# Kernel optimization log

Measured on AMD Instinct MI355X. Metric: run time of the kernel, lower is better.

## Reference

```python
import jax, jax.numpy as jnp
import numpy as np

B, S, D = 16, 2048, 128

def setup_inputs() -> dict:
    key = jax.random.key(0)
    kq, kk, kv, km = jax.random.split(key, 4)
    Q = jax.random.normal(kq, (B, S, D), dtype=jnp.float32)
    K = jax.random.normal(kk, (B, S, D), dtype=jnp.float32)
    V = jax.random.normal(kv, (B, S, D), dtype=jnp.float32)
    # mask: True entries are masked out (filled with -inf), same as torch.masked_fill_
    mask = jax.random.randint(km, (B, S, S), 0, 2).astype(bool)
    return {"Q": Q, "K": K, "V": V, "mask": mask, "dk": 128}

def reference(Q, K, V, mask, dk):
    # scores: [B, S_q, S_k]
    w = jnp.einsum('bqd,bkd->bqk', Q, K)
    w = jnp.where(mask, -jnp.inf, w)
    # scale applied to masked scores (as in original: mask first, then divide);
    # -inf / scale stays -inf, so math matches exactly.
    scale = jnp.asarray(dk, w.dtype) ** 0.5
    p = jax.nn.softmax(w / scale, axis=-1)
    # context: [B, S_q, D]
    return jnp.einsum('bqk,bkd->bqd', p, V)
```

## Files before the change

### kernel.cpp

```cpp
#include <hip/hip_runtime.h>
#include <hip/hip_bf16.h>
#include <stdint.h>

typedef __attribute__((ext_vector_type(8)))  short short8;
typedef __attribute__((ext_vector_type(4)))  float floatx4;
typedef __attribute__((ext_vector_type(16))) float floatx16;

#define S_LEN 2048
#define DH    128
#define BQ    64
#define BKV   64
#define NSTEP (S_LEN / BKV)
#define SCALE 0.08838834764831845f
#define SCALE2 0.12753785429791905f
#define DTHR 11.541560327111708f

__device__ __forceinline__ float ex2(float x) { return __builtin_amdgcn_exp2f(x); }

__device__ __forceinline__ unsigned short f2b(float f) {
    union { float f; unsigned u; } v; v.f = f;
    unsigned r = v.u + 0x7fffu + ((v.u >> 16) & 1u);
    return (unsigned short)(r >> 16);
}

__device__ __forceinline__ unsigned cvt_pk(float lo, float hi) {
    unsigned r;
    asm("v_cvt_pk_bf16_f32 %0, %1, %2" : "=v"(r) : "v"(lo), "v"(hi));
    return r;
}


__global__ __launch_bounds__(256) void kfrag_make(const float* __restrict__ K,
                                                  unsigned short* __restrict__ KF)
{
    const int T = blockIdx.x, b = blockIdx.y;
    const float* Kb = K + ((size_t)b * S_LEN + T * 64) * DH;
    unsigned short* out = KF + ((size_t)(b * 32 + T)) * 1024 * 8;
    #pragma unroll
    for (int i = 0; i < 4; ++i) {
        int F = i * 256 + threadIdx.x;
        int lq = F & 31, h = (F >> 5) & 1, dsub = (F >> 6) & 7, wk = F >> 9;
        const float* src = Kb + (size_t)(wk * 32 + lq) * DH + dsub * 16 + h * 8;
        float4 a = *(const float4*)src, bb = *(const float4*)(src + 4);
        short8 f;
        f[0] = f2b(a.x);  f[1] = f2b(a.y);  f[2] = f2b(a.z);  f[3] = f2b(a.w);
        f[4] = f2b(bb.x); f[5] = f2b(bb.y); f[6] = f2b(bb.z); f[7] = f2b(bb.w);
        *(short8*)(out + (size_t)F * 8) = f;
    }
}

__global__ __launch_bounds__(256) void vfrag_make(const float* __restrict__ V,
                                                  unsigned short* __restrict__ VF)
{
    __shared__ float t[32][33];
    const int k0 = blockIdx.x * 32, d0 = blockIdx.y * 32, b = blockIdx.z;
    const int tx = threadIdx.x & 31, ty = threadIdx.x >> 5;
    const float* Vb = V + ((size_t)b * S_LEN + k0) * DH + d0;
    #pragma unroll
    for (int i = 0; i < 4; ++i)
        t[ty + 8 * i][tx] = Vb[(size_t)(ty + 8 * i) * DH + tx];
    __syncthreads();
    if (threadIdx.x < 128) {
        const int lq = threadIdx.x & 31;
        const int h  = (threadIdx.x >> 5) & 1;
        const int ks = threadIdx.x >> 6;
        const int T = k0 >> 6, wk = (k0 >> 5) & 1, ds = d0 >> 5;
        short8 f;
        #pragma unroll
        for (int e = 0; e < 8; ++e)
            f[e] = f2b(t[ks * 16 + h * 8 + e][lq]);
        unsigned short* o = VF +
            ((((((size_t)(b * 32 + T) * 4 + ds) * 2 + wk) * 2 + ks) * 2 + h) * 32 + lq) * 8;
        *(short8*)o = f;
    }
}

#define PM_OFF 34816
#define LDS_BYTES 45056

__global__ __launch_bounds__(256, 2)
void attn_fwd(const float* __restrict__ Q, const unsigned short* __restrict__ KF,
              const unsigned short* __restrict__ VF,
              const int* __restrict__ M,
              float* __restrict__ O)
{
    __shared__ __align__(128) char lds[LDS_BYTES];

    const int tid  = threadIdx.x;
    const int lane = tid & 63;
    const int w    = tid >> 6;
    const int wq   = w & 1;
    const int wk   = w >> 1;
    const int lq   = lane & 31;
    const int hi   = lane >> 5;
    const int qt   = blockIdx.x;
    const int b    = blockIdx.y;
    const int q0   = qt * BQ;

    short8 qf[8];
    {
        const float* qrow = Q + ((size_t)(b * S_LEN + q0 + wq * 32 + lq)) * DH;
        #pragma unroll
        for (int dsub = 0; dsub < 8; ++dsub) {
            const float* p = qrow + dsub * 16 + hi * 8;
            float4 a  = *(const float4*)(p);
            float4 bb = *(const float4*)(p + 4);
            short8 f;
            f[0] = f2b(a.x * SCALE2);  f[1] = f2b(a.y * SCALE2);
            f[2] = f2b(a.z * SCALE2);  f[3] = f2b(a.w * SCALE2);
            f[4] = f2b(bb.x * SCALE2); f[5] = f2b(bb.y * SCALE2);
            f[6] = f2b(bb.z * SCALE2); f[7] = f2b(bb.w * SCALE2);
            qf[dsub] = f;
        }
    }

    float m_run = -1e30f;
    float l_run = 0.f;
    floatx16 accO[4];
    #pragma unroll
    for (int i = 0; i < 4; ++i) accO[i] = (floatx16)(0.f);

    const unsigned short* KFl = KF + (((size_t)(b * 32) * 2 + wk) * 512
                                      + (size_t)hi * 32 + lq) * 8;
    const unsigned short* VFl = VF + ((((size_t)(b * 32) * 4 * 2 + wk) * 2) * 2 * 32
                                      + (size_t)hi * 32 + lq) * 8;

    const int* Mq = M + (size_t)b * S_LEN * S_LEN + (size_t)q0 * S_LEN;

    int4 mA[4], mB[4];
    short8 kfc[8], vfc[8];
    unsigned long long mgc[4];

#define LOAD_KF(T) {                                                          \
    const unsigned short* kp_ = KFl + (size_t)(T) * (2 * 512 * 8);            \
    _Pragma("unroll")                                                         \
    for (int dsub = 0; dsub < 8; ++dsub)                                      \
        kfc[dsub] = *(const short8*)(kp_ + dsub * 512);                       \
}

#define LOAD_VF(T) {                                                          \
    _Pragma("unroll")                                                         \
    for (int ds = 0; ds < 4; ++ds)                                            \
        _Pragma("unroll")                                                     \
        for (int ks = 0; ks < 2; ++ks)                                        \
            vfc[ds * 2 + ks] = *(const short8*)(VFl                           \
                + ((size_t)(T) * 16 + ds * 4 + ks) * (2 * 32 * 8));           \
}

#define LOAD_MROWS(DST, G, SB) {                                              \
    _Pragma("unroll")                                                         \
    for (int rr = 0; rr < 4; ++rr)                                            \
        DST[rr] = *(const int4*)(Mq + (size_t)(w * 16 + (SB) * 4 + rr) * S_LEN \
                                 + (G) * 256 + 4 * lane);                     \
}
#define PACK_MROWS(SRC, PBUF, SB) {                                           \
    char* pms_ = lds + PM_OFF + (PBUF) * 2560;                                \
    _Pragma("unroll")                                                         \
    for (int rr = 0; rr < 4; ++rr) {                                          \
        int4 mm = SRC[rr];                                                    \
        unsigned long long b0 = __ballot(mm.x != 0);                          \
        unsigned long long b1 = __ballot(mm.y != 0);                          \
        unsigned long long b2 = __ballot(mm.z != 0);                          \
        unsigned long long b3 = __ballot(mm.w != 0);                          \
        if (lane == 0) {                                                      \
            char* rp_ = pms_ + (w * 16 + (SB) * 4 + rr) * 40;                 \
            *(unsigned long long*)(rp_ +  0) = b0;                            \
            *(unsigned long long*)(rp_ +  8) = b1;                            \
            *(unsigned long long*)(rp_ + 16) = b2;                            \
            *(unsigned long long*)(rp_ + 24) = b3;                            \
        }                                                                     \
    }                                                                         \
}

    #pragma unroll
    for (int gg = 0; gg < 2; ++gg)
        #pragma unroll
        for (int sb = 0; sb < 4; ++sb) {
            int4 t_[4];
            LOAD_MROWS(t_, gg, sb)
            PACK_MROWS(t_, gg, sb)
        }
    __syncthreads();

#define STEP_BODY(T, TT, MNEW, MOLD) {                                        \
    LOAD_KF(T);                                                               \
    LOAD_VF(T);                                                               \
               \
    if ((T) < 24) LOAD_MROWS(MNEW, ((T) >> 2) + 2, TT)                        \
                                     \
    if ((T) >= 1 && (T) <= 24) {                                              \
        const int ps_   = ((T) - 1) & 3;                                      \
        const int pbuf_ = (((((T) - 1) >> 2) + 2) & 3);                       \
        PACK_MROWS(MOLD, pbuf_, ps_)                                          \
    }                                                                         \
                   \
    if ((TT) == 0) {                                                          \
        const char* pmb_ = lds + PM_OFF + (((T) >> 2) & 3) * 2560             \
                           + (wq * 32 + lq) * 40;                             \
        mgc[0] = *(const unsigned long long*)(pmb_ + 0);                      \
        mgc[1] = *(const unsigned long long*)(pmb_ + 8);                      \
        mgc[2] = *(const unsigned long long*)(pmb_ + 16);                     \
        mgc[3] = *(const unsigned long long*)(pmb_ + 24);                     \
    }                                                                         \
                                                                    \
    floatx16 accS = (floatx16)(0.f);                                          \
    __builtin_amdgcn_s_setprio(1);                                            \
    _Pragma("unroll")                                                         \
    for (int dsub = 0; dsub < 8; ++dsub)                                      \
        accS = __builtin_amdgcn_mfma_f32_32x32x16_bf16(                       \
                   kfc[dsub], qf[dsub], accS, 0, 0, 0);                       \
    __builtin_amdgcn_s_setprio(0);                                            \
                    \
    const int base_ = (TT) * 16 + wk * 8 + hi;                                \
    unsigned mb0 = (unsigned)(mgc[0] >> base_);                               \
    unsigned mb1 = (unsigned)(mgc[1] >> base_);                               \
    unsigned mb2 = (unsigned)(mgc[2] >> base_);                               \
    unsigned mb3 = (unsigned)(mgc[3] >> base_);                               \
    float p_[16];                                                             \
    _Pragma("unroll")                                                         \
    for (int j = 0; j < 4; ++j) {                                             \
        p_[4*j+0] = ((mb0 >> (2*j)) & 1u) ? -1e30f : accS[4*j+0];             \
        p_[4*j+1] = ((mb1 >> (2*j)) & 1u) ? -1e30f : accS[4*j+1];             \
        p_[4*j+2] = ((mb2 >> (2*j)) & 1u) ? -1e30f : accS[4*j+2];             \
        p_[4*j+3] = ((mb3 >> (2*j)) & 1u) ? -1e30f : accS[4*j+3];             \
    }                                                                         \
    float mx = p_[0];                                                         \
    _Pragma("unroll")                                                         \
    for (int r = 1; r < 16; ++r) mx = fmaxf(mx, p_[r]);                       \
    mx = fmaxf(mx, __shfl_xor(mx, 32));                                       \
    int need = __any(mx - m_run > DTHR);                                      \
    float corr = 1.0f;                                                        \
    if (need) {                                                               \
        float mn = fmaxf(m_run, mx);                                          \
        corr = ex2(m_run - mn);                                               \
        m_run = mn;                                                           \
    }                                                                         \
    float ts = 0.f;                                                           \
    _Pragma("unroll")                                                         \
    for (int r = 0; r < 16; ++r) { p_[r] = ex2(p_[r] - m_run); ts += p_[r]; } \
    ts += __shfl_xor(ts, 32);                                                 \
    if (need) {                                                               \
        l_run = l_run * corr + ts;                                            \
        _Pragma("unroll")                                                     \
        for (int ds = 0; ds < 4; ++ds) {                                      \
            floatx16 o = accO[ds];                                            \
            _Pragma("unroll")                                                 \
            for (int r = 0; r < 16; ++r) o[r] *= corr;                        \
            accO[ds] = o;                                                     \
        }                                                                     \
    } else {                                                                  \
        l_run += ts;                                                          \
    }                                                                         \
                                 \
    short8 pf[2];                                                             \
    _Pragma("unroll")                                                         \
    for (int ks = 0; ks < 2; ++ks) {                                          \
        unsigned a01 = cvt_pk(p_[8*ks+0], p_[8*ks+1]);                        \
        unsigned a23 = cvt_pk(p_[8*ks+2], p_[8*ks+3]);                        \
        unsigned b01 = cvt_pk(p_[8*ks+4], p_[8*ks+5]);                        \
        unsigned b23 = cvt_pk(p_[8*ks+6], p_[8*ks+7]);                        \
        unsigned ta01 = (unsigned)__shfl_xor((int)a01, 32);                   \
        unsigned ta23 = (unsigned)__shfl_xor((int)a23, 32);                   \
        unsigned tb01 = (unsigned)__shfl_xor((int)b01, 32);                   \
        unsigned tb23 = (unsigned)__shfl_xor((int)b23, 32);                   \
        union { unsigned u[4]; short8 v; } pu;                                \
        pu.u[0] = hi ? tb01 : a01;                                            \
        pu.u[1] = hi ? tb23 : a23;                                            \
        pu.u[2] = hi ? b01 : ta01;                                            \
        pu.u[3] = hi ? b23 : ta23;                                            \
        pf[ks] = pu.v;                                                        \
    }                                                                         \
                                                                      \
    __builtin_amdgcn_s_setprio(1);                                            \
    _Pragma("unroll")                                                         \
    for (int ds = 0; ds < 4; ++ds)                                            \
        _Pragma("unroll")                                                     \
        for (int ks = 0; ks < 2; ++ks)                                        \
            accO[ds] = __builtin_amdgcn_mfma_f32_32x32x16_bf16(               \
                           vfc[ds * 2 + ks], pf[ks], accO[ds], 0, 0, 0);      \
    __builtin_amdgcn_s_setprio(0);                                            \
            \
    if ((TT) == 3) {                                                          \
        asm volatile("s_waitcnt lgkmcnt(0)" ::: "memory");                    \
        __builtin_amdgcn_s_barrier();                                         \
    }                                                                         \
}

    for (int g = 0; g < 8; ++g) {
        STEP_BODY(4 * g + 0, 0, mA, mB)
        STEP_BODY(4 * g + 1, 1, mB, mA)
        STEP_BODY(4 * g + 2, 2, mA, mB)
        STEP_BODY(4 * g + 3, 3, mB, mA)
    }
#undef STEP_BODY
#undef LOAD_KF
#undef LOAD_VF
#undef LOAD_MROWS
#undef PACK_MROWS

    {
        float* mg = (float*)lds;
        const int slot = (wq * 64 + lane) * 68;
        if (wk == 1) {
            #pragma unroll
            for (int ds = 0; ds < 4; ++ds)
                #pragma unroll
                for (int rr = 0; rr < 4; ++rr) {
                    float4 v;
                    v.x = accO[ds][4*rr+0]; v.y = accO[ds][4*rr+1];
                    v.z = accO[ds][4*rr+2]; v.w = accO[ds][4*rr+3];
                    *(float4*)(mg + slot + ds * 16 + rr * 4) = v;
                }
            mg[slot + 64] = m_run;
            mg[slot + 65] = l_run;
        }
        __syncthreads();
        if (wk == 0) {
            float m1 = mg[slot + 64], l1 = mg[slot + 65];
            float m  = fmaxf(m_run, m1);
            float f0 = ex2(m_run - m), f1 = ex2(m1 - m);
            float l  = l_run * f0 + l1 * f1;
            float inv = (l > 0.f) ? 1.f / l : 0.f;
            float* Ob = O + ((size_t)(b * S_LEN + q0 + wq * 32 + lq)) * DH;
            #pragma unroll
            for (int ds = 0; ds < 4; ++ds)
                #pragma unroll
                for (int rr = 0; rr < 4; ++rr) {
                    float4 part = *(const float4*)(mg + slot + ds * 16 + rr * 4);
                    float4 ov;
                    ov.x = (accO[ds][4*rr+0] * f0 + part.x * f1) * inv;
                    ov.y = (accO[ds][4*rr+1] * f0 + part.y * f1) * inv;
                    ov.z = (accO[ds][4*rr+2] * f0 + part.z * f1) * inv;
                    ov.w = (accO[ds][4*rr+3] * f0 + part.w * f1) * inv;
                    *(float4*)(Ob + ds * 32 + 8 * rr + 4 * hi) = ov;
                }
        }
    }
}

#define FB_LDS_BYTES 77824

__global__ __launch_bounds__(256, 2)
void attn_fwd_fb(const float* __restrict__ Q, const float* __restrict__ K,
                 const float* __restrict__ V, const int* __restrict__ M,
                 float* __restrict__ O)
{
    __shared__ __align__(128) char lds[FB_LDS_BYTES];

    const int tid  = threadIdx.x;
    const int lane = tid & 63;
    const int w    = tid >> 6;
    const int c    = lane & 15;
    const int g    = lane >> 4;
    const int qt   = blockIdx.x;
    const int b    = blockIdx.y;
    const int q0   = qt * 64;

    const int rbase = tid >> 5;
    const int c4    = tid & 31;
    const unsigned swk = (unsigned)(c4 * 8) ^ (unsigned)(rbase << 4);
    const int vd    = tid & 127;
    const int vk0   = (tid >> 7) * 32;

    short8 qf[4];
    {
        const float* qrow = Q + ((size_t)(b * S_LEN + q0 + w * 16 + c)) * DH;
        #pragma unroll
        for (int dk = 0; dk < 4; ++dk) {
            const float* p = qrow + dk * 32 + g * 8;
            float4 a  = *(const float4*)(p);
            float4 bb = *(const float4*)(p + 4);
            short8 f;
            f[0] = f2b(a.x * SCALE);  f[1] = f2b(a.y * SCALE);
            f[2] = f2b(a.z * SCALE);  f[3] = f2b(a.w * SCALE);
            f[4] = f2b(bb.x * SCALE); f[5] = f2b(bb.y * SCALE);
            f[6] = f2b(bb.z * SCALE); f[7] = f2b(bb.w * SCALE);
            qf[dk] = f;
        }
    }

    float m_run[4] = {-1e30f, -1e30f, -1e30f, -1e30f};
    float l_run[4] = {0.f, 0.f, 0.f, 0.f};
    floatx4 accO[8];
    #pragma unroll
    for (int i = 0; i < 8; ++i) accO[i] = (floatx4)(0.f);

    const float* Kb = K + (size_t)b * S_LEN * DH;
    const float* Vb = V + (size_t)b * S_LEN * DH;
    const int*   Mb = M + (size_t)b * S_LEN * S_LEN + (size_t)q0 * S_LEN;

    size_t moff[4];
    #pragma unroll
    for (int r = 0; r < 4; ++r)
        moff[r] = (size_t)(w * 16 + 4 * g + r) * S_LEN;

    float4 kreg[8];
    float  vreg[32];
    int    mreg[16];

    #pragma unroll
    for (int i = 0; i < 8; ++i)
        kreg[i] = *(const float4*)(Kb + (size_t)(i * 8 + rbase) * DH + c4 * 4);
    #pragma unroll
    for (int j = 0; j < 32; ++j)
        vreg[j] = Vb[(size_t)(vk0 + j) * DH + vd];
    #pragma unroll
    for (int r = 0; r < 4; ++r)
        #pragma unroll
        for (int n = 0; n < 4; ++n)
            mreg[r * 4 + n] = Mb[moff[r] + n * 16 + c];

    #pragma unroll
    for (int i = 0; i < 8; ++i) {
        float4 kv = kreg[i];
        unsigned long long kp =
              (unsigned long long)f2b(kv.x)
            | ((unsigned long long)f2b(kv.y) << 16)
            | ((unsigned long long)f2b(kv.z) << 32)
            | ((unsigned long long)f2b(kv.w) << 48);
        *(unsigned long long*)(lds + (i * 8 + rbase) * 256 + swk) = kp;
    }
    {
        char* vbase = lds + 32768 + vd * 144 + vk0 * 2;
        #pragma unroll
        for (int i = 0; i < 4; ++i) {
            short8 pk;
            #pragma unroll
            for (int e = 0; e < 8; ++e) pk[e] = f2b(vreg[i * 8 + e]);
            *(short8*)(vbase + i * 16) = pk;
        }
    }
    #pragma unroll
    for (int i = 0; i < 8; ++i)
        kreg[i] = *(const float4*)(Kb + (size_t)(BKV + i * 8 + rbase) * DH + c4 * 4);
    #pragma unroll
    for (int j = 0; j < 32; ++j)
        vreg[j] = Vb[(size_t)(BKV + vk0 + j) * DH + vd];

    __syncthreads();

    char* psw = lds + 69632 + w * 2048;

    for (int step = 0; step < NSTEP; ++step) {
        const int p = step & 1;
        const int kv0 = step * BKV;
        char* KHp = lds + p * 16384;
        char* VTp = lds + 32768 + p * 18432;

        floatx4 accS[4];
        #pragma unroll
        for (int n = 0; n < 4; ++n) accS[n] = (floatx4)(0.f);
        #pragma unroll
        for (int n = 0; n < 4; ++n) {
            const char* krow = KHp + (n * 16 + c) * 256;
            #pragma unroll
            for (int dk = 0; dk < 4; ++dk) {
                unsigned colb = (unsigned)(dk * 64 + g * 16) ^ (unsigned)((c & 7) << 4);
                short8 kf = *(const short8*)(krow + colb);
                accS[n] = __builtin_amdgcn_mfma_f32_16x16x32_bf16(qf[dk], kf, accS[n], 0, 0, 0);
            }
        }

        float pv[4][4];
        float corr[4];
        #pragma unroll
        for (int r = 0; r < 4; ++r) {
            float sv[4];
            #pragma unroll
            for (int n = 0; n < 4; ++n) {
                float s = accS[n][r];
                if (mreg[r * 4 + n]) s = -1e30f;
                sv[n] = s;
            }
            float tm = fmaxf(fmaxf(sv[0], sv[1]), fmaxf(sv[2], sv[3]));
            #pragma unroll
            for (int off = 1; off < 16; off <<= 1)
                tm = fmaxf(tm, __shfl_xor(tm, off, 64));
            float mn = fmaxf(m_run[r], tm);
            corr[r]  = __expf(m_run[r] - mn);
            m_run[r] = mn;
            float ts = 0.f;
            #pragma unroll
            for (int n = 0; n < 4; ++n) { pv[n][r] = __expf(sv[n] - mn); ts += pv[n][r]; }
            #pragma unroll
            for (int off = 1; off < 16; off <<= 1)
                ts += __shfl_xor(ts, off, 64);
            l_run[r] = l_run[r] * corr[r] + ts;
        }
        if (step + 1 < NSTEP) {
            const int kvn = kv0 + BKV;
            #pragma unroll
            for (int r = 0; r < 4; ++r)
                #pragma unroll
                for (int n = 0; n < 4; ++n)
                    mreg[r * 4 + n] = Mb[moff[r] + kvn + n * 16 + c];
        }

        #pragma unroll
        for (int s8 = 0; s8 < 8; ++s8) {
            floatx4 o = accO[s8];
            o[0] *= corr[0]; o[1] *= corr[1]; o[2] *= corr[2]; o[3] *= corr[3];
            accO[s8] = o;
        }

        #pragma unroll
        for (int r = 0; r < 4; ++r) {
            int rl = 4 * g + r;
            #pragma unroll
            for (int n = 0; n < 4; ++n) {
                unsigned colb = (unsigned)((n * 16 + c) * 2) ^ (unsigned)((rl & 7) << 4);
                *(unsigned short*)(psw + rl * 128 + colb) = f2b(pv[n][r]);
            }
        }

        #pragma unroll
        for (int sub = 0; sub < 2; ++sub) {
            unsigned colb = (unsigned)(sub * 64 + g * 16) ^ (unsigned)((c & 7) << 4);
            short8 pf = *(const short8*)(psw + c * 128 + colb);
            #pragma unroll
            for (int s8 = 0; s8 < 8; ++s8) {
                short8 vf = *(const short8*)(VTp + (s8 * 16 + c) * 144 + sub * 64 + g * 16);
                accO[s8] = __builtin_amdgcn_mfma_f32_16x16x32_bf16(pf, vf, accO[s8], 0, 0, 0);
            }
        }

        if (step + 1 < NSTEP) {
            char* KHn = lds + (p ^ 1) * 16384;
            char* VTn = lds + 32768 + (p ^ 1) * 18432;
            #pragma unroll
            for (int i = 0; i < 8; ++i) {
                float4 kv = kreg[i];
                unsigned long long kp =
                      (unsigned long long)f2b(kv.x)
                    | ((unsigned long long)f2b(kv.y) << 16)
                    | ((unsigned long long)f2b(kv.z) << 32)
                    | ((unsigned long long)f2b(kv.w) << 48);
                *(unsigned long long*)(KHn + (i * 8 + rbase) * 256 + swk) = kp;
            }
            char* vbase = VTn + vd * 144 + vk0 * 2;
            #pragma unroll
            for (int i = 0; i < 4; ++i) {
                short8 pk;
                #pragma unroll
                for (int e = 0; e < 8; ++e) pk[e] = f2b(vreg[i * 8 + e]);
                *(short8*)(vbase + i * 16) = pk;
            }
            if (step + 2 < NSTEP) {
                const int kvn2 = kv0 + 2 * BKV;
                #pragma unroll
                for (int i = 0; i < 8; ++i)
                    kreg[i] = *(const float4*)(Kb + (size_t)(kvn2 + i * 8 + rbase) * DH + c4 * 4);
                #pragma unroll
                for (int j = 0; j < 32; ++j)
                    vreg[j] = Vb[(size_t)(kvn2 + vk0 + j) * DH + vd];
            }
        }
        __syncthreads();
    }

    float inv[4];
    #pragma unroll
    for (int r = 0; r < 4; ++r) inv[r] = (l_run[r] > 0.f) ? 1.f / l_run[r] : 0.f;
    float* Ob = O + ((size_t)(b * S_LEN + q0 + w * 16)) * DH;
    #pragma unroll
    for (int s8 = 0; s8 < 8; ++s8) {
        #pragma unroll
        for (int r = 0; r < 4; ++r) {
            Ob[(size_t)(4 * g + r) * DH + s8 * 16 + c] = accO[s8][r] * inv[r];
        }
    }
}

extern "C" void kernel_launch(void* const* d_in, const int* in_sizes, int n_in,
                              void* d_out, int out_size, void* d_ws, size_t ws_size,
                              hipStream_t stream) {
    const float* Q = (const float*)d_in[0];
    const float* K = (const float*)d_in[1];
    const float* V = (const float*)d_in[2];
    const int*   M = (const int*)d_in[3];
    float*       O = (float*)d_out;

    const size_t elems    = (size_t)16 * S_LEN * DH;
    const size_t kv_bytes = elems * sizeof(unsigned short);
    if (ws_size >= 2 * kv_bytes) {
        unsigned short* KFp = (unsigned short*)d_ws;
        unsigned short* VFp = (unsigned short*)d_ws + elems;
        kfrag_make<<<dim3(32, 16), dim3(256), 0, stream>>>(K, KFp);
        vfrag_make<<<dim3(S_LEN / 32, DH / 32, 16), dim3(256), 0, stream>>>(V, VFp);
        attn_fwd<<<dim3(S_LEN / BQ, 16), dim3(256), 0, stream>>>(Q, KFp, VFp, M, O);
    } else {
        attn_fwd_fb<<<dim3(S_LEN / 64, 16), dim3(256), 0, stream>>>(Q, K, V, M, O);
    }
}
```

Measured before the change: 113.5 us.

## Split KV sequence across two blocks per query tile and merge partials

Adds a split-KV variant of the attention kernel. Each query tile's 2048 keys are divided between two blocks (blockIdx.z), and each block writes an unnormalized partial output plus its running max and sum to workspace. A separate merge kernel then combines the two partials with online-softmax rescaling. The aim is to double the grid size so more CUs are busy. The cost is roughly 32MB of extra partial-output traffic, an extra kernel launch, and a larger workspace requirement, with the old path kept as a fallback.

```diff
diff --git a/kernel.cpp b/kernel.cpp
--- a/kernel.cpp
+++ b/kernel.cpp
@@ -75,16 +75,15 @@
     }
 }
 
-#define PM_OFF 34816
-#define LDS_BYTES 45056
-
-__global__ __launch_bounds__(256, 2)
-void attn_fwd(const float* __restrict__ Q, const unsigned short* __restrict__ KF,
-              const unsigned short* __restrict__ VF,
-              const int* __restrict__ M,
-              float* __restrict__ O)
+#define SP_LDS 34816
+
+__global__ __launch_bounds__(256)
+void attn_split(const float* __restrict__ Q, const unsigned short* __restrict__ KF,
+                const unsigned short* __restrict__ VF,
+                const int* __restrict__ M,
+                float* __restrict__ OP, float* __restrict__ ML)
 {
-    __shared__ __align__(128) char lds[LDS_BYTES];
+    __shared__ __align__(128) char lds[SP_LDS];
 
     const int tid  = threadIdx.x;
     const int lane = tid & 63;
@@ -95,6 +94,7 @@
     const int hi   = lane >> 5;
     const int qt   = blockIdx.x;
     const int b    = blockIdx.y;
+    const int zh   = blockIdx.z;
     const int q0   = qt * BQ;
 
     short8 qf[8];
@@ -137,7 +137,6 @@
     for (int dsub = 0; dsub < 8; ++dsub)                                      \
         kfc[dsub] = *(const short8*)(kp_ + dsub * 512);                       \
 }
-
 #define LOAD_VF(T) {                                                          \
     _Pragma("unroll")                                                         \
     for (int ds = 0; ds < 4; ++ds)                                            \
@@ -146,15 +145,14 @@
             vfc[ds * 2 + ks] = *(const short8*)(VFl                           \
                 + ((size_t)(T) * 16 + ds * 4 + ks) * (2 * 32 * 8));           \
 }
-
 #define LOAD_MROWS(DST, G, SB) {                                              \
     _Pragma("unroll")                                                         \
     for (int rr = 0; rr < 4; ++rr)                                            \
         DST[rr] = *(const int4*)(Mq + (size_t)(w * 16 + (SB) * 4 + rr) * S_LEN \
-                                 + (G) * 256 + 4 * lane);                     \
+                                 + (size_t)(G) * 256 + 4 * lane);             \
 }
 #define PACK_MROWS(SRC, PBUF, SB) {                                           \
-    char* pms_ = lds + PM_OFF + (PBUF) * 2560;                                \
+    char* pms_ = lds + (PBUF) * 2560;                                         \
     _Pragma("unroll")                                                         \
     for (int rr = 0; rr < 4; ++rr) {                                          \
         int4 mm = SRC[rr];                                                    \
@@ -177,32 +175,27 @@
         #pragma unroll
         for (int sb = 0; sb < 4; ++sb) {
             int4 t_[4];
-            LOAD_MROWS(t_, gg, sb)
+            LOAD_MROWS(t_, zh * 4 + gg, sb)
             PACK_MROWS(t_, gg, sb)
         }
     __syncthreads();
 
-#define STEP_BODY(T, TT, MNEW, MOLD) {                                        \
+#define STEP_BODY(K, MCUR, MOLD) {                                            \
+    const int lt = 4 * g + (K);                                               \
+    const int T  = zh * 16 + lt;                                              \
     LOAD_KF(T);                                                               \
     LOAD_VF(T);                                                               \
-               \
-    if ((T) < 24) LOAD_MROWS(MNEW, ((T) >> 2) + 2, TT)                        \
-                                     \
-    if ((T) >= 1 && (T) <= 24) {                                              \
-        const int ps_   = ((T) - 1) & 3;                                      \
-        const int pbuf_ = (((((T) - 1) >> 2) + 2) & 3);                       \
-        PACK_MROWS(MOLD, pbuf_, ps_)                                          \
-    }                                                                         \
-                   \
-    if ((TT) == 0) {                                                          \
-        const char* pmb_ = lds + PM_OFF + (((T) >> 2) & 3) * 2560             \
-                           + (wq * 32 + lq) * 40;                             \
+    if (lt < 8) LOAD_MROWS(MCUR, zh * 4 + g + 2, K)                           \
+    if (lt >= 1 && lt <= 8) {                                                 \
+        PACK_MROWS(MOLD, ((((lt - 1) >> 2) + 2) & 3), ((lt - 1) & 3))         \
+    }                                                                         \
+    if ((K) == 0) {                                                           \
+        const char* pmb_ = lds + (g & 3) * 2560 + (wq * 32 + lq) * 40;        \
         mgc[0] = *(const unsigned long long*)(pmb_ + 0);                      \
         mgc[1] = *(const unsigned long long*)(pmb_ + 8);                      \
         mgc[2] = *(const unsigned long long*)(pmb_ + 16);                     \
         mgc[3] = *(const unsigned long long*)(pmb_ + 24);                     \
     }                                                                         \
-                                                                    \
     floatx16 accS = (floatx16)(0.f);                                          \
     __builtin_amdgcn_s_setprio(1);                                            \
     _Pragma("unroll")                                                         \
@@ -210,8 +203,7 @@
         accS = __builtin_amdgcn_mfma_f32_32x32x16_bf16(                       \
                    kfc[dsub], qf[dsub], accS, 0, 0, 0);                       \
     __builtin_amdgcn_s_setprio(0);                                            \
-                    \
-    const int base_ = (TT) * 16 + wk * 8 + hi;                                \
+    const int base_ = (K) * 16 + wk * 8 + hi;                                 \
     unsigned mb0 = (unsigned)(mgc[0] >> base_);                               \
     unsigned mb1 = (unsigned)(mgc[1] >> base_);                               \
     unsigned mb2 = (unsigned)(mgc[2] >> base_);                               \
@@ -251,7 +243,6 @@
     } else {                                                                  \
         l_run += ts;                                                          \
     }                                                                         \
-                                 \
     short8 pf[2];                                                             \
     _Pragma("unroll")                                                         \
     for (int ks = 0; ks < 2; ++ks) {                                          \
@@ -270,7 +261,6 @@
         pu.u[3] = hi ? b23 : ta23;                                            \
         pf[ks] = pu.v;                                                        \
     }                                                                         \
-                                                                      \
     __builtin_amdgcn_s_setprio(1);                                            \
     _Pragma("unroll")                                                         \
     for (int ds = 0; ds < 4; ++ds)                                            \
@@ -279,18 +269,17 @@
             accO[ds] = __builtin_amdgcn_mfma_f32_32x32x16_bf16(               \
                            vfc[ds * 2 + ks], pf[ks], accO[ds], 0, 0, 0);      \
     __builtin_amdgcn_s_setprio(0);                                            \
-            \
-    if ((TT) == 3) {                                                          \
+    if ((K) == 3) {                                                           \
         asm volatile("s_waitcnt lgkmcnt(0)" ::: "memory");                    \
         __builtin_amdgcn_s_barrier();                                         \
     }                                                                         \
 }
 
-    for (int g = 0; g < 8; ++g) {
-        STEP_BODY(4 * g + 0, 0, mA, mB)
-        STEP_BODY(4 * g + 1, 1, mB, mA)
-        STEP_BODY(4 * g + 2, 2, mA, mB)
-        STEP_BODY(4 * g + 3, 3, mB, mA)
+    for (int g = 0; g < 4; ++g) {
+        STEP_BODY(0, mA, mB)
+        STEP_BODY(1, mB, mA)
+        STEP_BODY(2, mA, mB)
+        STEP_BODY(3, mB, mA)
     }
 #undef STEP_BODY
 #undef LOAD_KF
@@ -316,9 +305,300 @@
         }
         __syncthreads();
         if (wk == 0) {
-            float m1 = mg[slot + 64], l1 = mg[slot + 65];
-            float m  = fmaxf(m_run, m1);
-            float f0 = ex2(m_run - m), f1 = ex2(m1 - m);
+            float m1v = mg[slot + 64], l1 = mg[slot + 65];
+            float m  = fmaxf(m_run, m1v);
+            float f0 = ex2(m_run - m), f1 = ex2(m1v - m);
+            float l  = l_run * f0 + l1 * f1;
+            const int pair = b * 32 + qt;
+            const int qrow = wq * 32 + lq;
+            float* Op = OP + ((size_t)(pair * 2 + zh) * 64 + qrow) * 128;
+            #pragma unroll
+            for (int ds = 0; ds < 4; ++ds)
+                #pragma unroll
+                for (int rr = 0; rr < 4; ++rr) {
+                    float4 part = *(const float4*)(mg + slot + ds * 16 + rr * 4);
+                    float4 ov;
+                    ov.x = accO[ds][4*rr+0] * f0 + part.x * f1;
+                    ov.y = accO[ds][4*rr+1] * f0 + part.y * f1;
+                    ov.z = accO[ds][4*rr+2] * f0 + part.z * f1;
+                    ov.w = accO[ds][4*rr+3] * f0 + part.w * f1;
+                    *(float4*)(Op + ds * 32 + 8 * rr + 4 * hi) = ov;
+                }
+            if (hi == 0) {
+                float* mlp = ML + ((size_t)(pair * 2 + zh) * 64 + qrow) * 2;
+                mlp[0] = m;
+                mlp[1] = l;
+            }
+        }
+    }
+}
+
+__global__ __launch_bounds__(256) void merge_o(const float* __restrict__ OP,
+                                               const float* __restrict__ ML,
+                                               float* __restrict__ O)
+{
+    const int pair = blockIdx.x;
+    const int qt = pair & 31, b = pair >> 5;
+    const int qrow = threadIdx.x >> 2;
+    const int c0   = (threadIdx.x & 3) * 32;
+    const float* mla = ML + ((size_t)(pair * 2 + 0) * 64 + qrow) * 2;
+    const float* mlb = ML + ((size_t)(pair * 2 + 1) * 64 + qrow) * 2;
+    float ma = mla[0], la = mla[1];
+    float mb = mlb[0], lb = mlb[1];
+    float m  = fmaxf(ma, mb);
+    float fa = ex2(ma - m), fb = ex2(mb - m);
+    float l  = la * fa + lb * fb;
+    float inv = (l > 0.f) ? 1.f / l : 0.f;
+    const float* Pa = OP + ((size_t)(pair * 2 + 0) * 64 + qrow) * 128 + c0;
+    const float* Pb = OP + ((size_t)(pair * 2 + 1) * 64 + qrow) * 128 + c0;
+    float* Ob = O + ((size_t)(b * S_LEN + qt * 64 + qrow)) * 128 + c0;
+    #pragma unroll
+    for (int j = 0; j < 8; ++j) {
+        float4 a = *(const float4*)(Pa + 4 * j);
+        float4 bv = *(const float4*)(Pb + 4 * j);
+        float4 o;
+        o.x = (a.x * fa + bv.x * fb) * inv;
+        o.y = (a.y * fa + bv.y * fb) * inv;
+        o.z = (a.z * fa + bv.z * fb) * inv;
+        o.w = (a.w * fa + bv.w * fb) * inv;
+        *(float4*)(Ob + 4 * j) = o;
+    }
+}
+
+#define PM_OFF 34816
+#define LDS_BYTES 45056
+
+__global__ __launch_bounds__(256, 2)
+void attn_fwd(const float* __restrict__ Q, const unsigned short* __restrict__ KF,
+              const unsigned short* __restrict__ VF,
+              const int* __restrict__ M,
+              float* __restrict__ O)
+{
+    __shared__ __align__(128) char lds[LDS_BYTES];
+
+    const int tid  = threadIdx.x;
+    const int lane = tid & 63;
+    const int w    = tid >> 6;
+    const int wq   = w & 1;
+    const int wk   = w >> 1;
+    const int lq   = lane & 31;
+    const int hi   = lane >> 5;
+    const int qt   = blockIdx.x;
+    const int b    = blockIdx.y;
+    const int q0   = qt * BQ;
+
+    short8 qf[8];
+    {
+        const float* qrow = Q + ((size_t)(b * S_LEN + q0 + wq * 32 + lq)) * DH;
+        #pragma unroll
+        for (int dsub = 0; dsub < 8; ++dsub) {
+            const float* p = qrow + dsub * 16 + hi * 8;
+            float4 a  = *(const float4*)(p);
+            float4 bb = *(const float4*)(p + 4);
+            short8 f;
+            f[0] = f2b(a.x * SCALE2);  f[1] = f2b(a.y * SCALE2);
+            f[2] = f2b(a.z * SCALE2);  f[3] = f2b(a.w * SCALE2);
+            f[4] = f2b(bb.x * SCALE2); f[5] = f2b(bb.y * SCALE2);
+            f[6] = f2b(bb.z * SCALE2); f[7] = f2b(bb.w * SCALE2);
+            qf[dsub] = f;
+        }
+    }
+
+    float m_run = -1e30f;
+    float l_run = 0.f;
+    floatx16 accO[4];
+    #pragma unroll
+    for (int i = 0; i < 4; ++i) accO[i] = (floatx16)(0.f);
+
+    const unsigned short* KFl = KF + (((size_t)(b * 32) * 2 + wk) * 512
+                                      + (size_t)hi * 32 + lq) * 8;
+    const unsigned short* VFl = VF + ((((size_t)(b * 32) * 4 * 2 + wk) * 2) * 2 * 32
+                                      + (size_t)hi * 32 + lq) * 8;
+
+    const int* Mq = M + (size_t)b * S_LEN * S_LEN + (size_t)q0 * S_LEN;
+
+    int4 mA[4], mB[4];
+    short8 kfc[8], vfc[8];
+    unsigned long long mgc[4];
+
+#define LOAD_KF(T) {                                                          \
+    const unsigned short* kp_ = KFl + (size_t)(T) * (2 * 512 * 8);            \
+    _Pragma("unroll")                                                         \
+    for (int dsub = 0; dsub < 8; ++dsub)                                      \
+        kfc[dsub] = *(const short8*)(kp_ + dsub * 512);                       \
+}
+#define LOAD_VF(T) {                                                          \
+    _Pragma("unroll")                                                         \
+    for (int ds = 0; ds < 4; ++ds)                                            \
+        _Pragma("unroll")                                                     \
+        for (int ks = 0; ks < 2; ++ks)                                        \
+            vfc[ds * 2 + ks] = *(const short8*)(VFl                           \
+                + ((size_t)(T) * 16 + ds * 4 + ks) * (2 * 32 * 8));           \
+}
+#define LOAD_MROWS(DST, G, SB) {                                              \
+    _Pragma("unroll")                                                         \
+    for (int rr = 0; rr < 4; ++rr)                                            \
+        DST[rr] = *(const int4*)(Mq + (size_t)(w * 16 + (SB) * 4 + rr) * S_LEN \
+                                 + (G) * 256 + 4 * lane);                     \
+}
+#define PACK_MROWS(SRC, PBUF, SB) {                                           \
+    char* pms_ = lds + PM_OFF + (PBUF) * 2560;                                \
+    _Pragma("unroll")                                                         \
+    for (int rr = 0; rr < 4; ++rr) {                                          \
+        int4 mm = SRC[rr];                                                    \
+        unsigned long long b0 = __ballot(mm.x != 0);                          \
+        unsigned long long b1 = __ballot(mm.y != 0);                          \
+        unsigned long long b2 = __ballot(mm.z != 0);                          \
+        unsigned long long b3 = __ballot(mm.w != 0);                          \
+        if (lane == 0) {                                                      \
+            char* rp_ = pms_ + (w * 16 + (SB) * 4 + rr) * 40;                 \
+            *(unsigned long long*)(rp_ +  0) = b0;                            \
+            *(unsigned long long*)(rp_ +  8) = b1;                            \
+            *(unsigned long long*)(rp_ + 16) = b2;                            \
+            *(unsigned long long*)(rp_ + 24) = b3;                            \
+        }                                                                     \
+    }                                                                         \
+}
+
+    #pragma unroll
+    for (int gg = 0; gg < 2; ++gg)
+        #pragma unroll
+        for (int sb = 0; sb < 4; ++sb) {
+            int4 t_[4];
+            LOAD_MROWS(t_, gg, sb)
+            PACK_MROWS(t_, gg, sb)
+        }
+    __syncthreads();
+
+#define STEP_BODY(T, TT, MCUR, MOLD) {                                        \
+    LOAD_KF(T);                                                               \
+    LOAD_VF(T);                                                               \
+    if ((T) < 24) LOAD_MROWS(MCUR, ((T) >> 2) + 2, TT)                        \
+    if ((T) >= 1 && (T) <= 24) {                                              \
+        const int ps_   = ((T) - 1) & 3;                                      \
+        const int pbuf_ = (((((T) - 1) >> 2) + 2) & 3);                       \
+        PACK_MROWS(MOLD, pbuf_, ps_)                                          \
+    }                                                                         \
+    if ((TT) == 0) {                                                          \
+        const char* pmb_ = lds + PM_OFF + (((T) >> 2) & 3) * 2560             \
+                           + (wq * 32 + lq) * 40;                             \
+        mgc[0] = *(const unsigned long long*)(pmb_ + 0);                      \
+        mgc[1] = *(const unsigned long long*)(pmb_ + 8);                      \
+        mgc[2] = *(const unsigned long long*)(pmb_ + 16);                     \
+        mgc[3] = *(const unsigned long long*)(pmb_ + 24);                     \
+    }                                                                         \
+    floatx16 accS = (floatx16)(0.f);                                          \
+    __builtin_amdgcn_s_setprio(1);                                            \
+    _Pragma("unroll")                                                         \
+    for (int dsub = 0; dsub < 8; ++dsub)                                      \
+        accS = __builtin_amdgcn_mfma_f32_32x32x16_bf16(                       \
+                   kfc[dsub], qf[dsub], accS, 0, 0, 0);                       \
+    __builtin_amdgcn_s_setprio(0);                                            \
+    const int base_ = (TT) * 16 + wk * 8 + hi;                                \
+    unsigned mb0 = (unsigned)(mgc[0] >> base_);                               \
+    unsigned mb1 = (unsigned)(mgc[1] >> base_);                               \
+    unsigned mb2 = (unsigned)(mgc[2] >> base_);                               \
+    unsigned mb3 = (unsigned)(mgc[3] >> base_);                               \
+    float p_[16];                                                             \
+    _Pragma("unroll")                                                         \
+    for (int j = 0; j < 4; ++j) {                                             \
+        p_[4*j+0] = ((mb0 >> (2*j)) & 1u) ? -1e30f : accS[4*j+0];             \
+        p_[4*j+1] = ((mb1 >> (2*j)) & 1u) ? -1e30f : accS[4*j+1];             \
+        p_[4*j+2] = ((mb2 >> (2*j)) & 1u) ? -1e30f : accS[4*j+2];             \
+        p_[4*j+3] = ((mb3 >> (2*j)) & 1u) ? -1e30f : accS[4*j+3];             \
+    }                                                                         \
+    float mx = p_[0];                                                         \
+    _Pragma("unroll")                                                         \
+    for (int r = 1; r < 16; ++r) mx = fmaxf(mx, p_[r]);                       \
+    mx = fmaxf(mx, __shfl_xor(mx, 32));                                       \
+    int need = __any(mx - m_run > DTHR);                                      \
+    float corr = 1.0f;                                                        \
+    if (need) {                                                               \
+        float mn = fmaxf(m_run, mx);                                          \
+        corr = ex2(m_run - mn);                                               \
+        m_run = mn;                                                           \
+    }                                                                         \
+    float ts = 0.f;                                                           \
+    _Pragma("unroll")                                                         \
+    for (int r = 0; r < 16; ++r) { p_[r] = ex2(p_[r] - m_run); ts += p_[r]; } \
+    ts += __shfl_xor(ts, 32);                                                 \
+    if (need) {                                                               \
+        l_run = l_run * corr + ts;                                            \
+        _Pragma("unroll")                                                     \
+        for (int ds = 0; ds < 4; ++ds) {                                      \
+            floatx16 o = accO[ds];                                            \
+            _Pragma("unroll")                                                 \
+            for (int r = 0; r < 16; ++r) o[r] *= corr;                        \
+            accO[ds] = o;                                                     \
+        }                                                                     \
+    } else {                                                                  \
+        l_run += ts;                                                          \
+    }                                                                         \
+    short8 pf[2];                                                             \
+    _Pragma("unroll")                                                         \
+    for (int ks = 0; ks < 2; ++ks) {                                          \
+        unsigned a01 = cvt_pk(p_[8*ks+0], p_[8*ks+1]);                        \
+        unsigned a23 = cvt_pk(p_[8*ks+2], p_[8*ks+3]);                        \
+        unsigned b01 = cvt_pk(p_[8*ks+4], p_[8*ks+5]);                        \
+        unsigned b23 = cvt_pk(p_[8*ks+6], p_[8*ks+7]);                        \
+        unsigned ta01 = (unsigned)__shfl_xor((int)a01, 32);                   \
+        unsigned ta23 = (unsigned)__shfl_xor((int)a23, 32);                   \
+        unsigned tb01 = (unsigned)__shfl_xor((int)b01, 32);                   \
+        unsigned tb23 = (unsigned)__shfl_xor((int)b23, 32);                   \
+        union { unsigned u[4]; short8 v; } pu;                                \
+        pu.u[0] = hi ? tb01 : a01;                                            \
+        pu.u[1] = hi ? tb23 : a23;                                            \
+        pu.u[2] = hi ? b01 : ta01;                                            \
+        pu.u[3] = hi ? b23 : ta23;                                            \
+        pf[ks] = pu.v;                                                        \
+    }                                                                         \
+    __builtin_amdgcn_s_setprio(1);                                            \
+    _Pragma("unroll")                                                         \
+    for (int ds = 0; ds < 4; ++ds)                                            \
+        _Pragma("unroll")                                                     \
+        for (int ks = 0; ks < 2; ++ks)                                        \
+            accO[ds] = __builtin_amdgcn_mfma_f32_32x32x16_bf16(               \
+                           vfc[ds * 2 + ks], pf[ks], accO[ds], 0, 0, 0);      \
+    __builtin_amdgcn_s_setprio(0);                                            \
+    if ((TT) == 3) {                                                          \
+        asm volatile("s_waitcnt lgkmcnt(0)" ::: "memory");                    \
+        __builtin_amdgcn_s_barrier();                                         \
+    }                                                                         \
+}
+
+    for (int g = 0; g < 8; ++g) {
+        STEP_BODY(4 * g + 0, 0, mA, mB)
+        STEP_BODY(4 * g + 1, 1, mB, mA)
+        STEP_BODY(4 * g + 2, 2, mA, mB)
+        STEP_BODY(4 * g + 3, 3, mB, mA)
+    }
+#undef STEP_BODY
+#undef LOAD_KF
+#undef LOAD_VF
+#undef LOAD_MROWS
+#undef PACK_MROWS
+
+    {
+        float* mg = (float*)lds;
+        const int slot = (wq * 64 + lane) * 68;
+        if (wk == 1) {
+            #pragma unroll
+            for (int ds = 0; ds < 4; ++ds)
+                #pragma unroll
+                for (int rr = 0; rr < 4; ++rr) {
+                    float4 v;
+                    v.x = accO[ds][4*rr+0]; v.y = accO[ds][4*rr+1];
+                    v.z = accO[ds][4*rr+2]; v.w = accO[ds][4*rr+3];
+                    *(float4*)(mg + slot + ds * 16 + rr * 4) = v;
+                }
+            mg[slot + 64] = m_run;
+            mg[slot + 65] = l_run;
+        }
+        __syncthreads();
+        if (wk == 0) {
+            float m1v = mg[slot + 64], l1 = mg[slot + 65];
+            float m  = fmaxf(m_run, m1v);
+            float f0 = ex2(m_run - m), f1 = ex2(m1v - m);
             float l  = l_run * f0 + l1 * f1;
             float inv = (l > 0.f) ? 1.f / l : 0.f;
             float* Ob = O + ((size_t)(b * S_LEN + q0 + wq * 32 + lq)) * DH;
@@ -582,7 +862,19 @@
 
     const size_t elems    = (size_t)16 * S_LEN * DH;
     const size_t kv_bytes = elems * sizeof(unsigned short);
-    if (ws_size >= 2 * kv_bytes) {
+    const size_t op_bytes = (size_t)1024 * 64 * 128 * sizeof(float);
+    const size_t ml_bytes = (size_t)1024 * 64 * 2 * sizeof(float);
+
+    if (ws_size >= 2 * kv_bytes + op_bytes + ml_bytes) {
+        unsigned short* KFp = (unsigned short*)d_ws;
+        unsigned short* VFp = (unsigned short*)d_ws + elems;
+        float* OP = (float*)((char*)d_ws + 2 * kv_bytes);
+        float* ML = (float*)((char*)d_ws + 2 * kv_bytes + op_bytes);
+        kfrag_make<<<dim3(32, 16), dim3(256), 0, stream>>>(K, KFp);
+        vfrag_make<<<dim3(S_LEN / 32, DH / 32, 16), dim3(256), 0, stream>>>(V, VFp);
+        attn_split<<<dim3(S_LEN / BQ, 16, 2), dim3(256), 0, stream>>>(Q, KFp, VFp, M, OP, ML);
+        merge_o<<<dim3(512), dim3(256), 0, stream>>>(OP, ML, O);
+    } else if (ws_size >= 2 * kv_bytes) {
         unsigned short* KFp = (unsigned short*)d_ws;
         unsigned short* VFp = (unsigned short*)d_ws + elems;
         kfrag_make<<<dim3(32, 16), dim3(256), 0, stream>>>(K, KFp);
```

Measured after the change: 170.7 us. +50.4%, slower.
